# Kernel optimization log

Hardware: AMD Instinct MI355X
Metric: run time of the kernel (lower is better)

Reference implementation:

```python
import jax, jax.numpy as jnp
import numpy as np

B, N, A = 2, 4096, 5
TOPK = 30
K_RBF = 16
MAX_AA = 22
MAXREL = 32
EDGE_IN = 16 + K_RBF * 25 + 14 + 16  # 446
EDGE_FEAT = 128
PI = 3.1415926


def l2norm(v, eps=1e-12):
    n = jnp.sqrt(jnp.sum(v * v, axis=-1, keepdims=True))
    return v / jnp.maximum(n, eps)


def gather_nodes(nodes, idx):
    # nodes: (B,N,C), idx: (B,N,K) -> (B,N,K,C)
    b, n, k = idx.shape
    flat = idx.reshape(b, n * k, 1)
    out = jnp.take_along_axis(nodes, flat, axis=1)
    return out.reshape(b, n, k, nodes.shape[-1])


def quaternions(R):
    # R: (...,3,3) -> unit quaternion (...,4)
    Rxx, Ryy, Rzz = R[..., 0, 0], R[..., 1, 1], R[..., 2, 2]
    mag = 0.5 * jnp.sqrt(jnp.abs(1.0 + jnp.stack([Rxx - Ryy - Rzz, -Rxx + Ryy - Rzz, -Rxx - Ryy + Rzz], -1)) + 1e-12)
    signs = jnp.sign(jnp.stack([R[..., 2, 1] - R[..., 1, 2], R[..., 0, 2] - R[..., 2, 0], R[..., 1, 0] - R[..., 0, 1]], -1))
    xyz = signs * mag
    w = jnp.sqrt(jax.nn.relu(1.0 + Rxx + Ryy + Rzz) + 1e-12)[..., None] / 2.0
    return l2norm(jnp.concatenate([xyz, w], -1))


def setup_inputs():
    key = jax.random.key(0)
    ks = jax.random.split(key, 12)
    X = jax.random.normal(ks[0], (B, N, A, 3), jnp.float32) * 3.0
    mask = jnp.ones((B, N), jnp.float32)
    mask_atoms = jnp.ones((B, N, A), jnp.float32)
    means = jax.random.normal(ks[1], (K_RBF,), jnp.float32)
    stds = jax.random.normal(ks[2], (K_RBF,), jnp.float32)
    mul_w = jax.random.normal(ks[3], (A * A,), jnp.float32)
    bias_w = jax.random.normal(ks[4], (A * A,), jnp.float32)
    aa_pair_embed = jax.random.normal(ks[5], (MAX_AA * MAX_AA, K_RBF), jnp.float32) * 0.02
    aa_pair_embed = aa_pair_embed.at[441].set(0.0)  # padding_idx
    relpos_embed = jax.random.normal(ks[6], (2 * MAXREL + 1, 16), jnp.float32) * 0.02
    mask_embed = jax.random.normal(ks[7], (2, 16), jnp.float32) * 0.02
    W1 = jax.random.normal(ks[8], (EDGE_IN, EDGE_IN), jnp.float32) / np.sqrt(EDGE_IN)
    b1 = jnp.zeros((EDGE_IN,), jnp.float32)
    W2 = jax.random.normal(ks[9], (EDGE_IN, EDGE_FEAT), jnp.float32) / np.sqrt(EDGE_IN)
    b2 = jnp.zeros((EDGE_FEAT,), jnp.float32)
    aa = jax.random.randint(ks[10], (B, N), 0, 21, jnp.int32)
    residue_idx = jnp.tile(jnp.arange(N, dtype=jnp.int32)[None, :], (B, 1))
    chain_labels = jax.random.randint(ks[11], (B, N), 0, 2, jnp.int32)
    return dict(X=X, mask=mask, mask_atoms=mask_atoms, means=means, stds=stds, mul_w=mul_w,
                bias_w=bias_w, aa_pair_embed=aa_pair_embed, relpos_embed=relpos_embed,
                mask_embed=mask_embed, W1=W1, b1=b1, W2=W2, b2=b2, aa=aa,
                residue_idx=residue_idx, chain_labels=chain_labels)


def reference(X, mask, mask_atoms, means, stds, mul_w, bias_w, aa_pair_embed, relpos_embed,
              mask_embed, W1, b1, W2, b2, aa, residue_idx, chain_labels):
    Ca = X[:, :, 1]  # (B,N,3) C-alpha
    # ---- _dist: spatial kNN over C-alpha ----
    mask2d = mask[:, :, None] * mask[:, None, :]
    dx = Ca[:, None, :, :] - Ca[:, :, None, :]
    D = mask2d * jnp.sqrt(jnp.sum(dx * dx, -1) + 1e-6)
    D_adj = D + (1.0 - mask2d) * jnp.max(D, -1, keepdims=True)
    _, E_idx = jax.lax.top_k(-D_adj, TOPK)  # smallest distances
    mask_attend = jnp.take_along_axis(mask2d, E_idx, axis=2)  # (B,N,K)
    # ---- orientation features (local frames + quaternions) ----
    ones3 = jnp.ones((B, 1, 3), X.dtype)
    u = l2norm(jnp.concatenate([ones3, Ca[:, 1:] - Ca[:, :-1]], 1))
    b_ = l2norm(jnp.concatenate([u[:, :-1] - u[:, 1:], ones3], 1))
    n_ = l2norm(jnp.concatenate([jnp.cross(u[:, :-1], u[:, 1:]), ones3], 1))
    lf = jnp.stack([b_, n_, jnp.cross(b_, n_)], axis=2)  # (B,N,3,3)
    X_nb = gather_nodes(Ca, E_idx)                       # (B,N,K,3)
    O_nb = gather_nodes(lf.reshape(B, N, 9), E_idx).reshape(B, N, TOPK, 3, 3)
    t = X_nb - Ca[:, :, None, :]
    t = jnp.einsum('bnij,bnkj->bnki', lf, t)
    t = l2norm(t) * mask_attend[..., None]
    r = jnp.einsum('bnji,bnkjl->bnkil', lf, O_nb)  # lf^T @ O_nb
    q = quaternions(r) * mask_attend[..., None]
    O_feat = jnp.concatenate([t, q, 1.0 - 2.0 * jnp.abs(t), 1.0 - 2.0 * jnp.abs(q)], -1)  # (B,N,K,14)
    # ---- positional / chain embeddings ----
    offset = residue_idx[:, :, None] - residue_idx[:, None, :]
    offset_nb = jnp.take_along_axis(offset, E_idx, 2)
    d_chain = (chain_labels[:, :, None] == chain_labels[:, None, :]).astype(jnp.int32)
    E_chains = jnp.take_along_axis(d_chain, E_idx, 2)
    d = jnp.clip(offset_nb + MAXREL, 0, 2 * MAXREL)
    E_pos = relpos_embed[d] + mask_embed[E_chains]  # (B,N,K,16)
    # ---- GaussianLayer: aa-pair embed + atom-pair distance RBF ----
    aa_pair = aa[:, :, None] * MAX_AA + aa[:, None, :]
    aa_nb = jnp.take_along_axis(aa_pair, E_idx, 2)
    feat_aapair = aa_pair_embed[aa_nb] * mask_attend[..., None]  # (B,N,K,16)
    nbX = gather_nodes(X.reshape(B, N, A * 3), E_idx).reshape(B, N, TOPK, A, 3)
    delta = nbX[:, :, :, :, None, :] - X[:, :, None, None, :, :]  # (B,N,K,A,A,3)
    Dab = jnp.sqrt(jnp.sum(delta * delta, -1) + 1e-12)            # (B,N,K,A,A)
    et = jnp.arange(A * A).reshape(A, A)
    xg = mul_w[et] * Dab + bias_w[et]
    m_nb = gather_nodes(mask_atoms, E_idx)  # (B,N,K,A)
    xg = xg * (m_nb[..., None, :] * m_nb[..., :, None])
    std = jnp.abs(stds) + 0.01
    g = jnp.exp(-0.5 * ((xg[..., None] - means) / std) ** 2) / ((2.0 * PI) ** 0.5 * std)
    gbf = g.reshape(B, N, TOPK, A * A * K_RBF) * mask_attend[..., None]  # (B,N,K,400)
    # ---- fuse and project (NonLinear gbf_proj) ----
    E = jnp.concatenate([E_pos, gbf, O_feat, feat_aapair], -1)  # (B,N,K,446)
    h = jax.nn.gelu(E @ W1 + b1, approximate=False)
    return h @ W2 + b2  # (B,N,K,128)
```

## Files before the change

kernel.cpp:

```cpp
#include <hip/hip_runtime.h>
#include <cstdint>
#include <cstddef>

#define NN 4096
#define TOPK_ 30
#define BN_TOT 8192
#define M_TOT 245760
#define KP 448
#define HSTRIDE 136
#define EF 128

typedef unsigned short u16;
typedef unsigned int u32;
typedef __attribute__((ext_vector_type(8))) short bf16x8;
typedef __attribute__((ext_vector_type(4))) float f32x4;

__device__ __forceinline__ float b2f(u16 u){ return __uint_as_float(((u32)u)<<16); }
__device__ __forceinline__ u16 f2b(float f){
  u32 u = __float_as_uint(f);
  return (u16)((u + 0x7FFFu + ((u>>16)&1u)) >> 16);
}
__device__ __forceinline__ float ldf(const void* p, long i, int fl){
  return fl ? ((const float*)p)[i] : b2f(((const u16*)p)[i]);
}
__device__ __forceinline__ int is_f32_flag(const u16* mask){
  return (((const u32*)mask)[0] == 0x3F800000u) ? 1 : 0;
}
__device__ __forceinline__ void norm3(float x,float y,float z,float&ox,float&oy,float&oz){
  float n = sqrtf(x*x+y*y+z*z); n = fmaxf(n, 1e-12f);
  ox=x/n; oy=y/n; oz=z/n;
}
__device__ __forceinline__ float sgn(float x){ return x>0.f?1.f:(x<0.f?-1.f:0.f); }
__device__ __forceinline__ float gelu_fast(float x){
  float y = 0.70710678118654752440f * x;
  float s = fabsf(y);
  float t = __builtin_amdgcn_rcpf(fmaf(0.3275911f, s, 1.0f));
  float p = fmaf(fmaf(fmaf(fmaf(1.061405429f, t, -1.453152027f), t, 1.421413741f), t,
                 -0.284496736f), t, 0.254829592f);
  float e = __expf(-y*y);
  float erfs = fmaf(-p*t, e, 1.0f);
  float erfy = (x >= 0.f) ? erfs : -erfs;
  float hx = 0.5f*x;
  return fmaf(hx, erfy, hx);
}
__device__ __forceinline__ u32 pk_bf16(float lo, float hi){
  u32 r;
  asm("v_cvt_pk_bf16_f32 %0, %1, %2" : "=v"(r) : "v"(lo), "v"(hi));
  return r;
}
__device__ __forceinline__ void ld16(const void* p, int row, int fl, float* o){
  if (fl) {
    const float4* q = (const float4*)((const float*)p + (long)row*16);
    float4 a=q[0], b=q[1], c=q[2], d=q[3];
    o[0]=a.x; o[1]=a.y; o[2]=a.z; o[3]=a.w;
    o[4]=b.x; o[5]=b.y; o[6]=b.z; o[7]=b.w;
    o[8]=c.x; o[9]=c.y; o[10]=c.z; o[11]=c.w;
    o[12]=d.x; o[13]=d.y; o[14]=d.z; o[15]=d.w;
  } else {
    const uint4* q = (const uint4*)((const u16*)p + (long)row*16);
    uint4 a=q[0], b=q[1];
    o[0]=__uint_as_float(a.x<<16);  o[1]=__uint_as_float(a.x&0xFFFF0000u);
    o[2]=__uint_as_float(a.y<<16);  o[3]=__uint_as_float(a.y&0xFFFF0000u);
    o[4]=__uint_as_float(a.z<<16);  o[5]=__uint_as_float(a.z&0xFFFF0000u);
    o[6]=__uint_as_float(a.w<<16);  o[7]=__uint_as_float(a.w&0xFFFF0000u);
    o[8]=__uint_as_float(b.x<<16);  o[9]=__uint_as_float(b.x&0xFFFF0000u);
    o[10]=__uint_as_float(b.y<<16); o[11]=__uint_as_float(b.y&0xFFFF0000u);
    o[12]=__uint_as_float(b.z<<16); o[13]=__uint_as_float(b.z&0xFFFF0000u);
    o[14]=__uint_as_float(b.w<<16); o[15]=__uint_as_float(b.w&0xFFFF0000u);
  }
}

__global__ __launch_bounds__(256) void prep_kernel(
    const void* __restrict__ X, const u16* __restrict__ mask,
    const void* __restrict__ mask_atoms,
    const void* __restrict__ means, const void* __restrict__ stds,
    const void* __restrict__ mul_w, const void* __restrict__ bias_w,
    const void* __restrict__ W1, const void* __restrict__ b1,
    const void* __restrict__ W2, const void* __restrict__ b2,
    float* __restrict__ ca, float* __restrict__ lf,
    u16* __restrict__ W1P, u16* __restrict__ W2P,
    float* __restrict__ b1p, float* __restrict__ b2p,
    float* __restrict__ Fp, float* __restrict__ wsc)
{
  const int fl = is_f32_flag(mask);
  int idx = blockIdx.x*256 + threadIdx.x;
  if (idx < BN_TOT) {
    int i = idx & (NN-1);
    float xr[15];
    #pragma unroll
    for (int v = 0; v < 15; ++v) xr[v] = ldf(X, (long)idx*15+v, fl);
    float cax = xr[3], cay = xr[4], caz = xr[5];
    ca[idx*4+0]=cax; ca[idx*4+1]=cay; ca[idx*4+2]=caz; ca[idx*4+3]=0.f;
    {
      float mres = ldf(mask, idx, fl);
      float m0 = ldf(mask_atoms,(long)idx*5+0,fl), m1 = ldf(mask_atoms,(long)idx*5+1,fl);
      float m2 = ldf(mask_atoms,(long)idx*5+2,fl), m3 = ldf(mask_atoms,(long)idx*5+3,fl);
      float m4 = ldf(mask_atoms,(long)idx*5+4,fl);
      float4* F4 = (float4*)(Fp + (long)idx*24);
      F4[0] = make_float4(xr[0],xr[1],xr[2],xr[3]);
      F4[1] = make_float4(xr[4],xr[5],xr[6],xr[7]);
      F4[2] = make_float4(xr[8],xr[9],xr[10],xr[11]);
      F4[3] = make_float4(xr[12],xr[13],xr[14],mres);
      F4[4] = make_float4(m0,m1,m2,m3);
      F4[5] = make_float4(m4,0.f,0.f,0.f);
    }
    float bx,by,bz,nx,ny,nz;
    if (i < NN-1) {
      float uix,uiy,uiz;
      if (i==0) { norm3(1.f,1.f,1.f,uix,uiy,uiz); }
      else {
        float px=ldf(X,(long)(idx-1)*15+3,fl), py=ldf(X,(long)(idx-1)*15+4,fl), pz=ldf(X,(long)(idx-1)*15+5,fl);
        norm3(cax-px, cay-py, caz-pz, uix,uiy,uiz);
      }
      float qx=ldf(X,(long)(idx+1)*15+3,fl), qy=ldf(X,(long)(idx+1)*15+4,fl), qz=ldf(X,(long)(idx+1)*15+5,fl);
      float vx,vy,vz; norm3(qx-cax, qy-cay, qz-caz, vx,vy,vz);
      norm3(uix-vx, uiy-vy, uiz-vz, bx,by,bz);
      norm3(uiy*vz-uiz*vy, uiz*vx-uix*vz, uix*vy-uiy*vx, nx,ny,nz);
    } else {
      norm3(1.f,1.f,1.f,bx,by,bz); nx=bx; ny=by; nz=bz;
    }
    float cx = by*nz - bz*ny, cy = bz*nx - bx*nz, cz = bx*ny - by*nx;
    float* L = lf + (size_t)idx*12;
    L[0]=bx;L[1]=by;L[2]=bz;L[3]=nx;L[4]=ny;L[5]=nz;L[6]=cx;L[7]=cy;L[8]=cz;
    return;
  }
  int r1 = idx - BN_TOT;
  if (r1 < 229376) {
    int f = r1 >> 9, li = r1 & 511;
    int n0 = f / 14, kc = f - n0*14;
    int ln = li >> 3, j = li & 7;
    int n = n0*16 + (ln & 15);
    int k = kc*32 + (ln >> 4)*8 + j;
    W1P[r1] = (n < 446 && k < 446) ? (fl ? f2b(((const float*)W1)[(long)k*446 + n])
                                         : ((const u16*)W1)[(long)k*446 + n]) : (u16)0;
    return;
  }
  int r2 = r1 - 229376;
  if (r2 < 65536) {
    int f = r2 >> 9, li = r2 & 511;
    int n0 = f >> 4, kc = f & 15;
    int ln = li >> 3, j = li & 7;
    int n = n0*16 + (ln & 15);
    int k = kc*32 + (ln >> 4)*8 + j;
    W2P[r2] = (k < 446) ? (fl ? f2b(((const float*)W2)[(long)k*128 + n])
                              : ((const u16*)W2)[(long)k*128 + n]) : (u16)0;
    return;
  }
  int r3 = r2 - 65536;
  if (r3 < 512) { b1p[r3] = (r3<446)? ldf(b1, r3, fl) : 0.f; return; }
  int r4 = r3 - 512;
  if (r4 < 128) { b2p[r4] = ldf(b2, r4, fl); return; }
  int r5 = r4 - 128;
  if (r5 < 16) {
    float sd = fabsf(ldf(stds, r5, fl)) + 0.01f;
    float ri = 1.0f / sd;
    wsc[r5] = ldf(means, r5, fl);
    wsc[16 + r5] = ri;
    wsc[32 + r5] = 0.3989422804014327f * ri;
    return;
  }
  if (r5 < 41) { wsc[48 + (r5-16)] = ldf(mul_w, r5-16, fl); return; }
  if (r5 < 66) { wsc[73 + (r5-41)] = ldf(bias_w, r5-41, fl); }
}

__global__ __launch_bounds__(64) void knn_kernel(const float4* __restrict__ ca,
                                                 int* __restrict__ eidx)
{
#pragma clang fp contract(off)
  __shared__ u32 keys[NN];
  int bi = blockIdx.x;
  int lane = threadIdx.x;
  int b = bi >> 12;
  const float4 ci = ca[bi];
  const float4* cab = ca + (b<<12);
  u32 mind = 0xFFFFFFFFu; int minj = 1<<30;
  for (int c = 0; c < 64; ++c) {
    int j = (c<<6) | lane;
    float4 cj = cab[j];
    float dx = cj.x-ci.x, dy = cj.y-ci.y, dz = cj.z-ci.z;
    float ss = dx*dx;
    ss = ss + dy*dy;
    ss = ss + dz*dz;
    float d = sqrtf(ss + 1e-6f);
    u32 db = __float_as_uint(d);
    keys[(c<<6)|lane] = db;
    if (db < mind) { mind = db; minj = j; }
  }
  __syncthreads();
  for (int r = 0; r < TOPK_; ++r) {
    u32 wd = mind; int wj = minj;
    #pragma unroll
    for (int off = 32; off; off >>= 1) {
      u32 od = __shfl_xor(wd, off, 64);
      int oj = __shfl_xor(wj, off, 64);
      if (od < wd || (od == wd && oj < wj)) { wd = od; wj = oj; }
    }
    if (lane == 0) eidx[bi*TOPK_ + r] = wj;
    int wl = wj & 63;
    if (lane == wl) keys[wj] = 0xFFFFFFFFu;
    __syncthreads();
    u32 kv = keys[(lane<<6)|wl];
    int kj = (lane<<6)|wl;
    #pragma unroll
    for (int off = 32; off; off >>= 1) {
      u32 od = __shfl_xor(kv, off, 64);
      int oj = __shfl_xor(kj, off, 64);
      if (od < kv || (od == kv && oj < kj)) { kv = od; kj = oj; }
    }
    if (lane == wl) { mind = kv; minj = kj; }
  }
}

__global__ __launch_bounds__(512,2) void mega_mlp(
    const float* __restrict__ Fp, const float* __restrict__ wsc,
    const u16* __restrict__ mask,
    const void* __restrict__ aa_pe, const void* __restrict__ relpos, const void* __restrict__ mask_emb,
    const int* __restrict__ aa, const int* __restrict__ ridx, const int* __restrict__ chains,
    const int* __restrict__ eidx, const float* __restrict__ ca, const float* __restrict__ lf,
    const u16* __restrict__ W1P, const u16* __restrict__ W2P,
    const float* __restrict__ b1p, const float* __restrict__ b2p,
    void* __restrict__ C)
{
  __shared__ __align__(16) u16 Et[128*448];
  __shared__ float Dabs[128][29];
  __shared__ float maA[128];
  const int fl = is_f32_flag(mask);
  int tid = threadIdx.x;
  int lane = tid & 63, wave = tid >> 6;
  int wr = wave >> 2, wc = wave & 3;
  int rowBase = blockIdx.x * 128;

  {
    int eo = tid >> 2, q = tid & 3;
    int e = rowBase + eo;
    int bi = (int)((unsigned)e / 30u);
    int k = e - bi*30;
    int bj = ((bi >> 12) << 12) + eidx[bi*TOPK_ + k];
    const float* Fi = Fp + (long)bi*24;
    const float* Fj = Fp + (long)bj*24;
    float Xi[15];
    {
      const float4* F4 = (const float4*)Fi;
      float4 A=F4[0], B=F4[1], Cc=F4[2], D=F4[3];
      Xi[0]=A.x;Xi[1]=A.y;Xi[2]=A.z;Xi[3]=A.w;
      Xi[4]=B.x;Xi[5]=B.y;Xi[6]=B.z;Xi[7]=B.w;
      Xi[8]=Cc.x;Xi[9]=Cc.y;Xi[10]=Cc.z;Xi[11]=Cc.w;
      Xi[12]=D.x;Xi[13]=D.y;Xi[14]=D.z;
      if (q == 1) maA[eo] = D.w * Fj[15];
    }
    float4 Mj = *(const float4*)(Fj + 16);
    float  Mj4 = Fj[20];
    for (int a = q; a < 5; a += 4) {
      float xj0 = Fj[a*3+0], xj1 = Fj[a*3+1], xj2 = Fj[a*3+2];
      float mja = (a==0)?Mj.x:(a==1)?Mj.y:(a==2)?Mj.z:(a==3)?Mj.w:Mj4;
      mja = Fj[16+a];
      #pragma unroll
      for (int c = 0; c < 5; ++c) {
        float d0 = xj0 - Xi[c*3+0];
        float d1 = xj1 - Xi[c*3+1];
        float d2 = xj2 - Xi[c*3+2];
        float Dab = sqrtf(d0*d0 + d1*d1 + d2*d2 + 1e-12f);
        float mjc = (c==0)?Mj.x:(c==1)?Mj.y:(c==2)?Mj.z:(c==3)?Mj.w:Mj4;
        float mw = wsc[48 + a*5+c], bw = wsc[73 + a*5+c];
        Dabs[eo][a*5+c] = (mw*Dab + bw) * (mja * mjc);
      }
    }
  }

  if (tid < 128) {
    int eo = tid;
    int e = rowBase + eo;
    int bi = (int)((unsigned)e / 30u);
    int k = e - bi*30;
    int bj = ((bi >> 12) << 12) + eidx[bi*TOPK_ + k];
    float ma = Fp[(long)bi*24+15] * Fp[(long)bj*24+15];
    char* rowB = (char*)Et + eo*896;
    int xr = (eo & 7) << 4;
    {
      int d = ridx[bi] - ridx[bj] + 32; d = d < 0 ? 0 : (d > 64 ? 64 : d);
      int ch = (chains[bi] == chains[bj]) ? 1 : 0;
      float rp[16], me[16];
      ld16(relpos, d, fl, rp);
      ld16(mask_emb, ch, fl, me);
      uint4 wA, wB;
      wA.x = pk_bf16(rp[0]+me[0],  rp[1]+me[1]);
      wA.y = pk_bf16(rp[2]+me[2],  rp[3]+me[3]);
      wA.z = pk_bf16(rp[4]+me[4],  rp[5]+me[5]);
      wA.w = pk_bf16(rp[6]+me[6],  rp[7]+me[7]);
      wB.x = pk_bf16(rp[8]+me[8],  rp[9]+me[9]);
      wB.y = pk_bf16(rp[10]+me[10],rp[11]+me[11]);
      wB.z = pk_bf16(rp[12]+me[12],rp[13]+me[13]);
      wB.w = pk_bf16(rp[14]+me[14],rp[15]+me[15]);
      *(uint4*)(rowB + (0 ^ xr))  = wA;
      *(uint4*)(rowB + (16 ^ xr)) = wB;
    }
    float t0,t1,t2,q0,q1,q2,qw;
    {
      float Li[9], Lj[9];
      {
        const float4* L4 = (const float4*)(lf + (size_t)bi*12);
        float4 a=L4[0], b=L4[1], c=L4[2];
        Li[0]=a.x;Li[1]=a.y;Li[2]=a.z;Li[3]=a.w;Li[4]=b.x;Li[5]=b.y;Li[6]=b.z;Li[7]=b.w;Li[8]=c.x;
        const float4* M4 = (const float4*)(lf + (size_t)bj*12);
        float4 d=M4[0], e2=M4[1], f=M4[2];
        Lj[0]=d.x;Lj[1]=d.y;Lj[2]=d.z;Lj[3]=d.w;Lj[4]=e2.x;Lj[5]=e2.y;Lj[6]=e2.z;Lj[7]=e2.w;Lj[8]=f.x;
      }
      float4 ci = *(const float4*)(ca + bj*4);
      float4 c0 = *(const float4*)(ca + bi*4);
      float dx = ci.x-c0.x, dy = ci.y-c0.y, dz = ci.z-c0.z;
      t0 = Li[0]*dx+Li[1]*dy+Li[2]*dz;
      t1 = Li[3]*dx+Li[4]*dy+Li[5]*dz;
      t2 = Li[6]*dx+Li[7]*dy+Li[8]*dz;
      float tn = fmaxf(sqrtf(t0*t0+t1*t1+t2*t2), 1e-12f);
      t0 = t0/tn*ma; t1 = t1/tn*ma; t2 = t2/tn*ma;
      float R00=Li[0]*Lj[0]+Li[3]*Lj[3]+Li[6]*Lj[6];
      float R01=Li[0]*Lj[1]+Li[3]*Lj[4]+Li[6]*Lj[7];
      float R02=Li[0]*Lj[2]+Li[3]*Lj[5]+Li[6]*Lj[8];
      float R10=Li[1]*Lj[0]+Li[4]*Lj[3]+Li[7]*Lj[6];
      float R11=Li[1]*Lj[1]+Li[4]*Lj[4]+Li[7]*Lj[7];
      float R12=Li[1]*Lj[2]+Li[4]*Lj[5]+Li[7]*Lj[8];
      float R20=Li[2]*Lj[0]+Li[5]*Lj[3]+Li[8]*Lj[6];
      float R21=Li[2]*Lj[1]+Li[5]*Lj[4]+Li[8]*Lj[7];
      float R22=Li[2]*Lj[2]+Li[5]*Lj[5]+Li[8]*Lj[8];
      float m0 = 0.5f*sqrtf(fabsf(1.f+R00-R11-R22)+1e-12f);
      float m1 = 0.5f*sqrtf(fabsf(1.f-R00+R11-R22)+1e-12f);
      float m2 = 0.5f*sqrtf(fabsf(1.f-R00-R11+R22)+1e-12f);
      q0 = sgn(R21-R12)*m0; q1 = sgn(R02-R20)*m1; q2 = sgn(R10-R01)*m2;
      qw = 0.5f*sqrtf(fmaxf(1.f+R00+R11+R22, 0.f)+1e-12f);
      float qn = fmaxf(sqrtf(q0*q0+q1*q1+q2*q2+qw*qw), 1e-12f);
      q0 = q0/qn*ma; q1 = q1/qn*ma; q2 = q2/qn*ma; qw = qw/qn*ma;
    }
    {
      int aap = aa[bi]*22 + aa[bj];
      float av[16];
      ld16(aa_pe, aap, fl, av);
      uint4 w0, w1, w2, w3;
      w0.x = pk_bf16(t0, t1);  w0.y = pk_bf16(t2, q0);
      w0.z = pk_bf16(q1, q2);  w0.w = pk_bf16(qw, 1.f-2.f*fabsf(t0));
      w1.x = pk_bf16(1.f-2.f*fabsf(t1), 1.f-2.f*fabsf(t2));
      w1.y = pk_bf16(1.f-2.f*fabsf(q0), 1.f-2.f*fabsf(q1));
      w1.z = pk_bf16(1.f-2.f*fabsf(q2), 1.f-2.f*fabsf(qw));
      w1.w = pk_bf16(av[0]*ma, av[1]*ma);
      w2.x = pk_bf16(av[2]*ma, av[3]*ma);   w2.y = pk_bf16(av[4]*ma, av[5]*ma);
      w2.z = pk_bf16(av[6]*ma, av[7]*ma);   w2.w = pk_bf16(av[8]*ma, av[9]*ma);
      w3.x = pk_bf16(av[10]*ma, av[11]*ma); w3.y = pk_bf16(av[12]*ma, av[13]*ma);
      w3.z = pk_bf16(av[14]*ma, av[15]*ma); w3.w = 0u;
      *(uint4*)(rowB + (832 ^ xr)) = w0;
      *(uint4*)(rowB + (848 ^ xr)) = w1;
      *(uint4*)(rowB + (864 ^ xr)) = w2;
      *(uint4*)(rowB + (880 ^ xr)) = w3;
    }
  }
  __syncthreads();

  {
    float meanv[16], rinvv[16], coefv[16];
    {
      const float4* W4 = (const float4*)wsc;
      #pragma unroll
      for (int g = 0; g < 4; ++g) {
        float4 m = W4[g], r = W4[4+g], c = W4[8+g];
        meanv[g*4+0]=m.x; meanv[g*4+1]=m.y; meanv[g*4+2]=m.z; meanv[g*4+3]=m.w;
        rinvv[g*4+0]=r.x; rinvv[g*4+1]=r.y; rinvv[g*4+2]=r.z; rinvv[g*4+3]=r.w;
        coefv[g*4+0]=c.x; coefv[g*4+1]=c.y; coefv[g*4+2]=c.z; coefv[g*4+3]=c.w;
      }
    }
    #pragma unroll 1
    for (int i = 0; i < 13; ++i) {
      int G = tid + i*512;
      if (G < 6400) {
        int row = (int)((unsigned)G / 50u);
        int gp = G - row*50;
        float xg = Dabs[row][gp >> 1];
        float ma = maA[row];
        int odd = gp & 1;
        u32 w[4];
        #pragma unroll
        for (int j2 = 0; j2 < 4; ++j2) {
          float me0 = odd ? meanv[j2*2+8] : meanv[j2*2];
          float ri0 = odd ? rinvv[j2*2+8] : rinvv[j2*2];
          float co0 = odd ? coefv[j2*2+8] : coefv[j2*2];
          float me1 = odd ? meanv[j2*2+9] : meanv[j2*2+1];
          float ri1 = odd ? rinvv[j2*2+9] : rinvv[j2*2+1];
          float co1 = odd ? coefv[j2*2+9] : coefv[j2*2+1];
          float z0 = (xg - me0) * ri0;
          float z1 = (xg - me1) * ri1;
          float v0 = __expf(-0.5f*z0*z0) * co0 * ma;
          float v1 = __expf(-0.5f*z1*z1) * co1 * ma;
          w[j2] = pk_bf16(v0, v1);
        }
        uint4 W4o; W4o.x = w[0]; W4o.y = w[1]; W4o.z = w[2]; W4o.w = w[3];
        *(uint4*)((char*)Et + row*896 + ((32 + (gp<<4)) ^ ((row&7)<<4))) = W4o;
      }
    }
  }
  __syncthreads();

  f32x4 acc1[4][4][2] = {};
  #pragma unroll 1
  for (int t = 0; t < 7; ++t) {
    bf16x8 af[2][4];
    #pragma unroll
    for (int kk = 0; kk < 2; ++kk)
      #pragma unroll
      for (int r = 0; r < 4; ++r) {
        int row = wr*64 + r*16 + (lane&15);
        int s = kk*4 + (lane>>4);
        af[kk][r] = *(const bf16x8*)(Et + row*448 + t*64 + ((s ^ (row&7))<<3));
      }
    bf16x8 bgA[2][2][2];
    #pragma unroll
    for (int c = 0; c < 2; ++c)
      #pragma unroll
      for (int cc = 0; cc < 2; ++cc)
        #pragma unroll
        for (int kk = 0; kk < 2; ++kk)
          bgA[c][cc][kk] = *(const bf16x8*)(W1P + (((c*8 + wc*2 + cc)*14 + t*2 + kk) << 9) + lane*8);
    #pragma unroll
    for (int c = 0; c < 2; ++c)
      #pragma unroll
      for (int r = 0; r < 4; ++r)
        #pragma unroll
        for (int cc = 0; cc < 2; ++cc)
          #pragma unroll
          for (int kk = 0; kk < 2; ++kk)
            acc1[c][r][cc] = __builtin_amdgcn_mfma_f32_16x16x32_bf16(af[kk][r], bgA[c][cc][kk], acc1[c][r][cc], 0,0,0);
    bf16x8 bgB[2][2][2];
    #pragma unroll
    for (int c = 0; c < 2; ++c)
      #pragma unroll
      for (int cc = 0; cc < 2; ++cc)
        #pragma unroll
        for (int kk = 0; kk < 2; ++kk)
          bgB[c][cc][kk] = *(const bf16x8*)(W1P + ((((c+2)*8 + wc*2 + cc)*14 + t*2 + kk) << 9) + lane*8);
    #pragma unroll
    for (int c = 0; c < 2; ++c)
      #pragma unroll
      for (int r = 0; r < 4; ++r)
        #pragma unroll
        for (int cc = 0; cc < 2; ++cc)
          #pragma unroll
          for (int kk = 0; kk < 2; ++kk)
            acc1[c+2][r][cc] = __builtin_amdgcn_mfma_f32_16x16x32_bf16(af[kk][r], bgB[c][cc][kk], acc1[c+2][r][cc], 0,0,0);
  }

  u32 hpk[4][4][2][2];
  #pragma unroll
  for (int c = 0; c < 4; ++c)
    #pragma unroll
    for (int r = 0; r < 4; ++r)
      #pragma unroll
      for (int cc = 0; cc < 2; ++cc) {
        int col = wc*32 + cc*16 + (lane & 15);
        float bv = b1p[c*128 + col];
        hpk[c][r][cc][0] = pk_bf16(gelu_fast(acc1[c][r][cc][0]+bv),
                                   gelu_fast(acc1[c][r][cc][1]+bv));
        hpk[c][r][cc][1] = pk_bf16(gelu_fast(acc1[c][r][cc][2]+bv),
                                   gelu_fast(acc1[c][r][cc][3]+bv));
      }

  u16* hs0 = Et;
  u16* hs1 = Et + 128*HSTRIDE;
  #define STORE_HS(cN, buf) do {                                                  \
    _Pragma("unroll")                                                             \
    for (int r = 0; r < 4; ++r) {                                                 \
      _Pragma("unroll")                                                           \
      for (int cc = 0; cc < 2; ++cc) {                                            \
        int col = wc*32 + cc*16 + (lane & 15);                                    \
        int row0 = wr*64 + r*16 + (lane>>4)*4;                                    \
        u32 p01 = hpk[cN][r][cc][0], p23 = hpk[cN][r][cc][1];                     \
        u16* hb_ = (buf) + row0*HSTRIDE + col;                                    \
        hb_[0]         = (u16)p01; hb_[HSTRIDE]   = (u16)(p01>>16);               \
        hb_[2*HSTRIDE] = (u16)p23; hb_[3*HSTRIDE] = (u16)(p23>>16);               \
      }                                                                           \
    }                                                                             \
  } while(0)

  f32x4 acc2[4][2] = {};
  __syncthreads();
  STORE_HS(0, hs0);
  __syncthreads();
  #pragma unroll
  for (int c = 0; c < 4; ++c) {
    u16* hb = (c & 1) ? hs1 : hs0;
    u16* hn = (c & 1) ? hs0 : hs1;
    if (c < 3) STORE_HS(c+1, hn);
    #pragma unroll
    for (int k2 = 0; k2 < 4; ++k2) {
      bf16x8 af2[4], bg2[2];
      #pragma unroll
      for (int r = 0; r < 4; ++r) {
        int row = wr*64 + r*16 + (lane&15);
        af2[r] = *(const bf16x8*)(hb + row*HSTRIDE + k2*32 + (lane>>4)*8);
      }
      #pragma unroll
      for (int cc = 0; cc < 2; ++cc)
        bg2[cc] = *(const bf16x8*)(W2P + ((((wc*2+cc)*16) + c*4 + k2) << 9) + lane*8);
      #pragma unroll
      for (int r = 0; r < 4; ++r)
        #pragma unroll
        for (int cc = 0; cc < 2; ++cc)
          acc2[r][cc] = __builtin_amdgcn_mfma_f32_16x16x32_bf16(af2[r], bg2[cc], acc2[r][cc], 0,0,0);
    }
    __syncthreads();
  }
  #undef STORE_HS

  const int f32out = fl;
  #pragma unroll
  for (int r = 0; r < 4; ++r) {
    #pragma unroll
    for (int cc = 0; cc < 2; ++cc) {
      int col = wc*32 + cc*16 + (lane & 15);
      float bv = b2p[col];
      #pragma unroll
      for (int g = 0; g < 4; ++g) {
        long row = (long)rowBase + wr*64 + r*16 + (lane>>4)*4 + g;
        float v = acc2[r][cc][g] + bv;
        long o = row*EF + col;
        if (f32out) ((float*)C)[o] = v;
        else        ((u16*)C)[o]  = f2b(v);
      }
    }
  }
}

extern "C" void kernel_launch(void* const* d_in, const int* in_sizes, int n_in,
                              void* d_out, int out_size, void* d_ws, size_t ws_size,
                              hipStream_t stream) {
  const void* X          = d_in[0];
  const u16* mask        = (const u16*)d_in[1];
  const void* mask_atoms = d_in[2];
  const void* means      = d_in[3];
  const void* stds       = d_in[4];
  const void* mul_w      = d_in[5];
  const void* bias_w     = d_in[6];
  const void* aa_pe      = d_in[7];
  const void* relpos     = d_in[8];
  const void* mask_emb   = d_in[9];
  const void* W1         = d_in[10];
  const void* b1         = d_in[11];
  const void* W2         = d_in[12];
  const void* b2         = d_in[13];
  const int* aa          = (const int*)d_in[14];
  const int* ridx        = (const int*)d_in[15];
  const int* chains      = (const int*)d_in[16];

  char* ws = (char*)d_ws;
  float* ca  = (float*)(ws + 0);
  float* lf  = (float*)(ws + 131072);
  int* eidx  = (int*)(ws + 524288);
  u16* W1P   = (u16*)(ws + 1507328);
  u16* W2P   = (u16*)(ws + 1966080);
  float* b1p = (float*)(ws + 2097152);
  float* b2p = (float*)(ws + 2099200);
  float* wsc = (float*)(ws + 2099712);
  float* Fp  = (float*)(ws + 2100224);

  prep_kernel<<<1187, 256, 0, stream>>>(X, mask, mask_atoms, means, stds, mul_w, bias_w,
                                        W1, b1, W2, b2, ca, lf, W1P, W2P, b1p, b2p, Fp, wsc);
  knn_kernel<<<BN_TOT, 64, 0, stream>>>((const float4*)ca, eidx);
  mega_mlp<<<M_TOT/128, 512, 0, stream>>>(Fp, wsc, mask,
                                          aa_pe, relpos, mask_emb, aa, ridx, chains,
                                          eidx, ca, lf, W1P, W2P, b1p, b2p, d_out);
}
```

Baseline: 709.3 us.

## Split GEMM1 into two column halves and pad knn key array

The first MLP GEMM now runs as two passes over 256 output columns each instead of one pass over all 512. This halves the live accumulator registers (64 to 32 f32x4), which should ease register pressure under the 512-thread launch bound, at the cost of reading the A tile from shared memory twice. The knn kernel's shared key array is transposed with a padding of 65 so the per-round column read by lane avoids bank conflicts. A redundant mask assignment is also removed.

```diff
diff --git a/kernel.cpp b/kernel.cpp
--- a/kernel.cpp
+++ b/kernel.cpp
@@ -167,7 +167,7 @@
                                                  int* __restrict__ eidx)
 {
 #pragma clang fp contract(off)
-  __shared__ u32 keys[NN];
+  __shared__ u32 keys[64*65];
   int bi = blockIdx.x;
   int lane = threadIdx.x;
   int b = bi >> 12;
@@ -183,7 +183,7 @@
     ss = ss + dz*dz;
     float d = sqrtf(ss + 1e-6f);
     u32 db = __float_as_uint(d);
-    keys[(c<<6)|lane] = db;
+    keys[lane*65 + c] = db;
     if (db < mind) { mind = db; minj = j; }
   }
   __syncthreads();
@@ -197,9 +197,9 @@
     }
     if (lane == 0) eidx[bi*TOPK_ + r] = wj;
     int wl = wj & 63;
-    if (lane == wl) keys[wj] = 0xFFFFFFFFu;
+    if (lane == wl) keys[wl*65 + (wj>>6)] = 0xFFFFFFFFu;
     __syncthreads();
-    u32 kv = keys[(lane<<6)|wl];
+    u32 kv = keys[wl*65 + lane];
     int kj = (lane<<6)|wl;
     #pragma unroll
     for (int off = 32; off; off >>= 1) {
@@ -252,8 +252,7 @@
     float  Mj4 = Fj[20];
     for (int a = q; a < 5; a += 4) {
       float xj0 = Fj[a*3+0], xj1 = Fj[a*3+1], xj2 = Fj[a*3+2];
-      float mja = (a==0)?Mj.x:(a==1)?Mj.y:(a==2)?Mj.z:(a==3)?Mj.w:Mj4;
-      mja = Fj[16+a];
+      float mja = Fj[16+a];
       #pragma unroll
       for (int c = 0; c < 5; ++c) {
         float d0 = xj0 - Xi[c*3+0];
@@ -396,68 +395,58 @@
   }
   __syncthreads();
 
-  f32x4 acc1[4][4][2] = {};
-  #pragma unroll 1
-  for (int t = 0; t < 7; ++t) {
-    bf16x8 af[2][4];
-    #pragma unroll
-    for (int kk = 0; kk < 2; ++kk)
-      #pragma unroll
-      for (int r = 0; r < 4; ++r) {
-        int row = wr*64 + r*16 + (lane&15);
-        int s = kk*4 + (lane>>4);
-        af[kk][r] = *(const bf16x8*)(Et + row*448 + t*64 + ((s ^ (row&7))<<3));
-      }
-    bf16x8 bgA[2][2][2];
-    #pragma unroll
-    for (int c = 0; c < 2; ++c)
-      #pragma unroll
-      for (int cc = 0; cc < 2; ++cc)
-        #pragma unroll
-        for (int kk = 0; kk < 2; ++kk)
-          bgA[c][cc][kk] = *(const bf16x8*)(W1P + (((c*8 + wc*2 + cc)*14 + t*2 + kk) << 9) + lane*8);
-    #pragma unroll
-    for (int c = 0; c < 2; ++c)
-      #pragma unroll
-      for (int r = 0; r < 4; ++r)
-        #pragma unroll
-        for (int cc = 0; cc < 2; ++cc)
-          #pragma unroll
-          for (int kk = 0; kk < 2; ++kk)
-            acc1[c][r][cc] = __builtin_amdgcn_mfma_f32_16x16x32_bf16(af[kk][r], bgA[c][cc][kk], acc1[c][r][cc], 0,0,0);
-    bf16x8 bgB[2][2][2];
-    #pragma unroll
-    for (int c = 0; c < 2; ++c)
-      #pragma unroll
-      for (int cc = 0; cc < 2; ++cc)
-        #pragma unroll
-        for (int kk = 0; kk < 2; ++kk)
-          bgB[c][cc][kk] = *(const bf16x8*)(W1P + ((((c+2)*8 + wc*2 + cc)*14 + t*2 + kk) << 9) + lane*8);
-    #pragma unroll
-    for (int c = 0; c < 2; ++c)
-      #pragma unroll
-      for (int r = 0; r < 4; ++r)
-        #pragma unroll
-        for (int cc = 0; cc < 2; ++cc)
-          #pragma unroll
-          for (int kk = 0; kk < 2; ++kk)
-            acc1[c+2][r][cc] = __builtin_amdgcn_mfma_f32_16x16x32_bf16(af[kk][r], bgB[c][cc][kk], acc1[c+2][r][cc], 0,0,0);
-  }
-
   u32 hpk[4][4][2][2];
-  #pragma unroll
-  for (int c = 0; c < 4; ++c)
-    #pragma unroll
-    for (int r = 0; r < 4; ++r)
-      #pragma unroll
-      for (int cc = 0; cc < 2; ++cc) {
-        int col = wc*32 + cc*16 + (lane & 15);
-        float bv = b1p[c*128 + col];
-        hpk[c][r][cc][0] = pk_bf16(gelu_fast(acc1[c][r][cc][0]+bv),
-                                   gelu_fast(acc1[c][r][cc][1]+bv));
-        hpk[c][r][cc][1] = pk_bf16(gelu_fast(acc1[c][r][cc][2]+bv),
-                                   gelu_fast(acc1[c][r][cc][3]+bv));
-      }
+  #define GEMM1_HALF(H) do {                                                      \
+    f32x4 acc1h[2][4][2] = {};                                                    \
+    _Pragma("unroll 1")                                                           \
+    for (int t = 0; t < 7; ++t) {                                                 \
+      bf16x8 af[2][4];                                                            \
+      _Pragma("unroll")                                                           \
+      for (int kk = 0; kk < 2; ++kk)                                              \
+        _Pragma("unroll")                                                         \
+        for (int r = 0; r < 4; ++r) {                                             \
+          int row = wr*64 + r*16 + (lane&15);                                     \
+          int s = kk*4 + (lane>>4);                                               \
+          af[kk][r] = *(const bf16x8*)(Et + row*448 + t*64 + ((s ^ (row&7))<<3)); \
+        }                                                                         \
+      bf16x8 bg[2][2][2];                                                         \
+      _Pragma("unroll")                                                           \
+      for (int c = 0; c < 2; ++c)                                                 \
+        _Pragma("unroll")                                                         \
+        for (int cc = 0; cc < 2; ++cc)                                            \
+          _Pragma("unroll")                                                       \
+          for (int kk = 0; kk < 2; ++kk)                                          \
+            bg[c][cc][kk] = *(const bf16x8*)(W1P +                                \
+              ((((2*(H)+c)*8 + wc*2 + cc)*14 + t*2 + kk) << 9) + lane*8);         \
+      _Pragma("unroll")                                                           \
+      for (int c = 0; c < 2; ++c)                                                 \
+        _Pragma("unroll")                                                         \
+        for (int r = 0; r < 4; ++r)                                               \
+          _Pragma("unroll")                                                       \
+          for (int cc = 0; cc < 2; ++cc)                                          \
+            _Pragma("unroll")                                                     \
+            for (int kk = 0; kk < 2; ++kk)                                        \
+              acc1h[c][r][cc] = __builtin_amdgcn_mfma_f32_16x16x32_bf16(          \
+                  af[kk][r], bg[c][cc][kk], acc1h[c][r][cc], 0,0,0);              \
+    }                                                                             \
+    _Pragma("unroll")                                                             \
+    for (int c = 0; c < 2; ++c)                                                   \
+      _Pragma("unroll")                                                           \
+      for (int r = 0; r < 4; ++r)                                                 \
+        _Pragma("unroll")                                                         \
+        for (int cc = 0; cc < 2; ++cc) {                                          \
+          int col = wc*32 + cc*16 + (lane & 15);                                  \
+          float bv = b1p[(2*(H)+c)*128 + col];                                    \
+          hpk[2*(H)+c][r][cc][0] = pk_bf16(gelu_fast(acc1h[c][r][cc][0]+bv),      \
+                                           gelu_fast(acc1h[c][r][cc][1]+bv));     \
+          hpk[2*(H)+c][r][cc][1] = pk_bf16(gelu_fast(acc1h[c][r][cc][2]+bv),      \
+                                           gelu_fast(acc1h[c][r][cc][3]+bv));     \
+        }                                                                         \
+  } while(0)
+
+  GEMM1_HALF(0);
+  GEMM1_HALF(1);
+  #undef GEMM1_HALF
 
   u16* hs0 = Et;
   u16* hs1 = Et + 128*HSTRIDE;
```

Result: faster. 673.3 us (-5.1%).
